# Kernel optimization log

Measured on AMD Instinct MI355X. Metric: run time of the kernel, lower is better.

Reference implementation:

```python
import jax, jax.numpy as jnp
import numpy as np

KAPPA = 5.0
EPS_NORM = 1e-12  # torch F.normalize eps
EPS_LOG = 1e-09


def setup_inputs() -> dict:
    key = jax.random.key(0)
    student_output = jax.random.normal(key, (16384, 256), dtype=jnp.float32)
    return {"student_output": student_output}


def reference(student_output) -> jnp.ndarray:
    # L2-normalize rows (matches F.normalize: x / max(||x||, eps))
    norm = jnp.linalg.norm(student_output, axis=-1, keepdims=True)
    x_norm = student_output / jnp.maximum(norm, EPS_NORM)
    # pairwise cosine similarity [n, n]
    sim = x_norm @ x_norm.T
    kernel = jnp.exp(KAPPA * sim)
    density_estimates = kernel.sum(axis=1)  # [n]
    entropy = -jnp.mean(jnp.log(density_estimates + EPS_LOG))
    return entropy
```

## Files before the change

kernel.cpp:

```cpp
#include <hip/hip_runtime.h>


#define NROWS 16384
#define KDIM 256
#define NTILE 128
#define NT (NROWS / NTILE)
#define NSTRIP 4
#define TOTAL_BLOCKS (NT * NSTRIP)

#define SQRT_KLOG2E 2.68579577857f

typedef int i32x4_t __attribute__((ext_vector_type(4)));
typedef int i32x8_t __attribute__((ext_vector_type(8)));
typedef float f32x16_t __attribute__((ext_vector_type(16)));
typedef __attribute__((address_space(1))) const void global_cvoid_t;
typedef __attribute__((address_space(3))) void lds_void_t;

#if __has_builtin(__builtin_amdgcn_exp2f)
#define EXP2(x) __builtin_amdgcn_exp2f(x)
#else
#define EXP2(x) exp2f(x)
#endif

union frag8 { i32x8_t v8; i32x4_t v4[2]; };

__global__ __launch_bounds__(256)
void kde_normalize(const float* __restrict__ X, unsigned int* __restrict__ Xn8,
                   float* __restrict__ density, unsigned int* __restrict__ ticket) {
  const int wave = threadIdx.x >> 6;
  const int lane = threadIdx.x & 63;
  const int row = blockIdx.x * 4 + wave;
  const float4 v = ((const float4*)(X + (size_t)row * KDIM))[lane];
  float ss = v.x * v.x + v.y * v.y + v.z * v.z + v.w * v.w;
  ss += __shfl_xor(ss, 1);
  ss += __shfl_xor(ss, 2);
  ss += __shfl_xor(ss, 4);
  ss += __shfl_xor(ss, 8);
  ss += __shfl_xor(ss, 16);
  ss += __shfl_xor(ss, 32);
  const float scale = SQRT_KLOG2E / fmaxf(sqrtf(ss), 1e-12f);
  int p = 0;
  p = __builtin_amdgcn_cvt_pk_fp8_f32(v.x * scale, v.y * scale, p, false);
  p = __builtin_amdgcn_cvt_pk_fp8_f32(v.z * scale, v.w * scale, p, true);
  Xn8[(size_t)row * 64 + lane] = (unsigned int)p;
  if (threadIdx.x < 4) density[blockIdx.x * 4 + threadIdx.x] = 0.0f;
  if (blockIdx.x == 0 && threadIdx.x == 0) *ticket = 0u;
}

__global__ __launch_bounds__(512, 4)
void kde_gemm(const unsigned char* __restrict__ Xn8, float* __restrict__ density,
              unsigned int* __restrict__ ticket, float* __restrict__ out) {
  extern __shared__ char smem[];
  char* buf0 = smem;
  char* buf1 = smem + 32768;

  const int tid = threadIdx.x;
  const int wave = tid >> 6;
  const int lane = tid & 63;
  const int wr = wave >> 1;
  const int wc = wave & 1;
  const int m32 = lane & 31;
  const int h = lane >> 5;
  const int bi = blockIdx.x;
  const int s = blockIdx.y;
  const int t0 = s * 16;
  const int nt = (s == 0 && bi < NT / 2) ? 17 : 16;
  const char* Xb = (const char*)Xn8;

#define STAGE(base_row, dst)                                                      \
  for (int c = wave; c < 32; c += 8) {                                            \
    const int rt = c >> 3, kb = (c >> 1) & 3, hh = c & 1;                         \
    const size_t gofs =                                                           \
        (size_t)((base_row) + rt * 32 + m32) * KDIM + kb * 64 + h * 32 + hh * 16; \
    __builtin_amdgcn_global_load_lds((global_cvoid_t*)(Xb + gofs),                \
                                     (lds_void_t*)((dst) + c * 1024), 16, 0, 0);  \
  }

  STAGE(bi * NTILE, buf0);
  STAGE(((bi + t0) & (NT - 1)) * NTILE, buf1);
  __syncthreads();

  frag8 areg[4];
#pragma unroll
  for (int kb = 0; kb < 4; kb++) {
    const char* pa = buf0 + (wr * 8 + kb * 2) * 1024 + lane * 16;
    areg[kb].v4[0] = *(const i32x4_t*)pa;
    areg[kb].v4[1] = *(const i32x4_t*)(pa + 1024);
  }
  __syncthreads();

  float rs[16];
#pragma unroll
  for (int r = 0; r < 16; r++) rs[r] = 0.0f;

  for (int k = 0; k < nt; ++k) {
    const int t = t0 + (k == 16 ? 48 : k) + (k == 16 ? 16 : 0);
    const int J = (bi + t) & (NT - 1);
    char* rbuf = (k & 1) ? buf0 : buf1;
    char* sbuf = (k & 1) ? buf1 : buf0;

    if (k + 1 < nt) {
      const int tn = t0 + (k + 1 == 16 ? 64 : k + 1);
      STAGE(((bi + tn) & (NT - 1)) * NTILE, sbuf);
    }

    f32x16_t acc[2];
#pragma unroll
    for (int j = 0; j < 2; j++) acc[j] = (f32x16_t)0.0f;

#pragma unroll
    for (int kb = 0; kb < 4; ++kb) {
      frag8 bf[2];
#pragma unroll
      for (int j = 0; j < 2; j++) {
        const char* pb = rbuf + ((wc * 2 + j) * 8 + kb * 2) * 1024 + lane * 16;
        bf[j].v4[0] = *(const i32x4_t*)pb;
        bf[j].v4[1] = *(const i32x4_t*)(pb + 1024);
      }
#pragma unroll
      for (int j = 0; j < 2; j++)
        acc[j] = __builtin_amdgcn_mfma_scale_f32_32x32x64_f8f6f4(
            areg[kb].v8, bf[j].v8, acc[j], 0, 0, 0, 127, 0, 127);
    }

    float cs[2] = {0.0f, 0.0f};
#pragma unroll
    for (int j = 0; j < 2; j++)
#pragma unroll
      for (int r = 0; r < 16; r++) {
        const float e = EXP2(acc[j][r]);
        rs[r] += e;
        cs[j] += e;
      }

    if (t != 0) {
#pragma unroll
      for (int j = 0; j < 2; j++) {
        float v = cs[j] + __shfl_xor(cs[j], 32);
        if (h == 0)
          atomicAdd(&density[J * NTILE + wc * 64 + j * 32 + m32], v);
      }
    }

    __syncthreads();
  }

#pragma unroll
  for (int r = 0; r < 16; r++) {
    float v = rs[r];
    v += __shfl_xor(v, 1);
    v += __shfl_xor(v, 2);
    v += __shfl_xor(v, 4);
    v += __shfl_xor(v, 8);
    v += __shfl_xor(v, 16);
    if (m32 == 0) {
      const int row = bi * NTILE + wr * 32 + (r & 3) + 8 * (r >> 2) + 4 * h;
      atomicAdd(&density[row], v);
    }
  }
#undef STAGE

  __syncthreads();
  if (tid == 0) {
    __threadfence();
    ((volatile unsigned int*)smem)[0] = atomicAdd(ticket, 1u);
  }
  __syncthreads();
  if (((volatile unsigned int*)smem)[0] == TOTAL_BLOCKS - 1) {
    __threadfence();
    float ssum = 0.0f;
    for (int i = tid; i < NROWS; i += 512) {
      const float d = __hip_atomic_load(&density[i], __ATOMIC_RELAXED,
                                        __HIP_MEMORY_SCOPE_AGENT);
      ssum += logf(d + 1e-9f);
    }
    ssum += __shfl_xor(ssum, 1);
    ssum += __shfl_xor(ssum, 2);
    ssum += __shfl_xor(ssum, 4);
    ssum += __shfl_xor(ssum, 8);
    ssum += __shfl_xor(ssum, 16);
    ssum += __shfl_xor(ssum, 32);
    float* red = ((float*)smem) + 16;
    if (lane == 0) red[wave] = ssum;
    __syncthreads();
    if (tid == 0) {
      float tot = 0.0f;
      for (int w = 0; w < 8; w++) tot += red[w];
      out[0] = -tot / (float)NROWS;
    }
  }
}

extern "C" void kernel_launch(void* const* d_in, const int* in_sizes, int n_in,
                              void* d_out, int out_size, void* d_ws, size_t ws_size,
                              hipStream_t stream) {
  const float* X = (const float*)d_in[0];
  float* out = (float*)d_out;
  char* ws = (char*)d_ws;
  unsigned int* Xn8 = (unsigned int*)ws;
  float* density = (float*)(ws + (size_t)NROWS * KDIM);
  unsigned int* ticket = (unsigned int*)(density + NROWS);

  hipFuncSetAttribute((const void*)kde_gemm,
                      hipFuncAttributeMaxDynamicSharedMemorySize, 65536);

  kde_normalize<<<NROWS / 4, 256, 0, stream>>>(X, Xn8, density, ticket);
  kde_gemm<<<dim3(NT, NSTRIP), 512, 65536, stream>>>((const unsigned char*)ws,
                                                     density, ticket, out);
}
```

Before: 124.7 us.

## Split tile staging into halves, buffer column sums in LDS, add MFMA priority

Each k-iteration now loads the next tile in two halves. Explicit vmcnt waits and raw barriers replace the full __syncthreads, so loads can overlap the MFMA and exp work. Per-tile column sums accumulate into an LDS buffer with LDS atomics and are flushed to global density once at the end, which removes the per-iteration global atomics. The change also adds s_setprio around the MFMAs and packs the row-sum accumulators as float2, at the cost of extra LDS and more delicate hand-written synchronisation.

```diff
diff --git a/kernel.cpp b/kernel.cpp
--- a/kernel.cpp
+++ b/kernel.cpp
@@ -10,8 +10,12 @@
 
 #define SQRT_KLOG2E 2.68579577857f
 
+#define CS_LDS_FLOATS (17 * NTILE)
+#define SMEM_BYTES (65536 + CS_LDS_FLOATS * 4)
+
 typedef int i32x4_t __attribute__((ext_vector_type(4)));
 typedef int i32x8_t __attribute__((ext_vector_type(8)));
+typedef float f32x2_t __attribute__((ext_vector_type(2)));
 typedef float f32x16_t __attribute__((ext_vector_type(16)));
 typedef __attribute__((address_space(1))) const void global_cvoid_t;
 typedef __attribute__((address_space(3))) void lds_void_t;
@@ -21,6 +25,8 @@
 #else
 #define EXP2(x) exp2f(x)
 #endif
+
+#define WAITVM(n) asm volatile("s_waitcnt vmcnt(" #n ")" ::: "memory")
 
 union frag8 { i32x8_t v8; i32x4_t v4[2]; };
 
@@ -53,6 +59,7 @@
   extern __shared__ char smem[];
   char* buf0 = smem;
   char* buf1 = smem + 32768;
+  float* cs_lds = (float*)(smem + 65536);
 
   const int tid = threadIdx.x;
   const int wave = tid >> 6;
@@ -76,6 +83,22 @@
                                      (lds_void_t*)((dst) + c * 1024), 16, 0, 0);  \
   }
 
+#define STAGE_HALF(base_row, dst, hf)                                             \
+  {                                                                               \
+    const int rt_ = wave >> 1;                                                    \
+    const int kb_ = 2 * (hf) + (wave & 1);                                        \
+    const size_t g0_ =                                                            \
+        (size_t)((base_row) + rt_ * 32 + m32) * KDIM + kb_ * 64 + h * 32;         \
+    __builtin_amdgcn_global_load_lds(                                             \
+        (global_cvoid_t*)(Xb + g0_),                                              \
+        (lds_void_t*)((dst) + (rt_ * 8 + kb_ * 2) * 1024), 16, 0, 0);             \
+    __builtin_amdgcn_global_load_lds(                                             \
+        (global_cvoid_t*)(Xb + g0_ + 16),                                         \
+        (lds_void_t*)((dst) + (rt_ * 8 + kb_ * 2 + 1) * 1024), 16, 0, 0);         \
+  }
+
+  for (int i = tid; i < nt * NTILE; i += 512) cs_lds[i] = 0.0f;
+
   STAGE(bi * NTILE, buf0);
   STAGE(((bi + t0) & (NT - 1)) * NTILE, buf1);
   __syncthreads();
@@ -89,65 +112,87 @@
   }
   __syncthreads();
 
-  float rs[16];
-#pragma unroll
-  for (int r = 0; r < 16; r++) rs[r] = 0.0f;
+  f32x2_t rs2[8];
+#pragma unroll
+  for (int r = 0; r < 8; r++) rs2[r] = (f32x2_t)0.0f;
 
   for (int k = 0; k < nt; ++k) {
-    const int t = t0 + (k == 16 ? 48 : k) + (k == 16 ? 16 : 0);
-    const int J = (bi + t) & (NT - 1);
+    const int t = (k == 16) ? 64 : (t0 + k);
     char* rbuf = (k & 1) ? buf0 : buf1;
     char* sbuf = (k & 1) ? buf1 : buf0;
-
-    if (k + 1 < nt) {
-      const int tn = t0 + (k + 1 == 16 ? 64 : k + 1);
-      STAGE(((bi + tn) & (NT - 1)) * NTILE, sbuf);
-    }
+    const bool pre = (k + 1 < nt);
+    const int tn = (k + 1 == 16) ? 64 : (t0 + k + 1);
+    const int Jn = (bi + tn) & (NT - 1);
 
     f32x16_t acc[2];
 #pragma unroll
     for (int j = 0; j < 2; j++) acc[j] = (f32x16_t)0.0f;
 
-#pragma unroll
-    for (int kb = 0; kb < 4; ++kb) {
+    if (pre) STAGE_HALF(Jn * NTILE, sbuf, 0);
+#pragma unroll
+    for (int kbl = 0; kbl < 2; ++kbl) {
       frag8 bf[2];
 #pragma unroll
       for (int j = 0; j < 2; j++) {
-        const char* pb = rbuf + ((wc * 2 + j) * 8 + kb * 2) * 1024 + lane * 16;
+        const char* pb = rbuf + ((wc * 2 + j) * 8 + kbl * 2) * 1024 + lane * 16;
         bf[j].v4[0] = *(const i32x4_t*)pb;
         bf[j].v4[1] = *(const i32x4_t*)(pb + 1024);
       }
+      __builtin_amdgcn_s_setprio(1);
 #pragma unroll
       for (int j = 0; j < 2; j++)
         acc[j] = __builtin_amdgcn_mfma_scale_f32_32x32x64_f8f6f4(
-            areg[kb].v8, bf[j].v8, acc[j], 0, 0, 0, 127, 0, 127);
-    }
-
-    float cs[2] = {0.0f, 0.0f};
-#pragma unroll
-    for (int j = 0; j < 2; j++)
-#pragma unroll
-      for (int r = 0; r < 16; r++) {
-        const float e = EXP2(acc[j][r]);
-        rs[r] += e;
-        cs[j] += e;
-      }
-
-    if (t != 0) {
+            areg[kbl].v8, bf[j].v8, acc[j], 0, 0, 0, 127, 0, 127);
+      __builtin_amdgcn_s_setprio(0);
+    }
+    if (pre) { WAITVM(2); } else { WAITVM(0); }
+    __builtin_amdgcn_s_barrier();
+
+    if (pre) STAGE_HALF(Jn * NTILE, sbuf, 1);
+#pragma unroll
+    for (int kbl = 0; kbl < 2; ++kbl) {
+      frag8 bf[2];
 #pragma unroll
       for (int j = 0; j < 2; j++) {
-        float v = cs[j] + __shfl_xor(cs[j], 32);
+        const char* pb =
+            rbuf + ((wc * 2 + j) * 8 + (2 + kbl) * 2) * 1024 + lane * 16;
+        bf[j].v4[0] = *(const i32x4_t*)pb;
+        bf[j].v4[1] = *(const i32x4_t*)(pb + 1024);
+      }
+      __builtin_amdgcn_s_setprio(1);
+#pragma unroll
+      for (int j = 0; j < 2; j++)
+        acc[j] = __builtin_amdgcn_mfma_scale_f32_32x32x64_f8f6f4(
+            areg[2 + kbl].v8, bf[j].v8, acc[j], 0, 0, 0, 127, 0, 127);
+      __builtin_amdgcn_s_setprio(0);
+    }
+
+#pragma unroll
+    for (int j = 0; j < 2; j++) {
+      f32x2_t csj = (f32x2_t)0.0f;
+#pragma unroll
+      for (int r2 = 0; r2 < 8; r2++) {
+        f32x2_t e;
+        e.x = EXP2(acc[j][2 * r2]);
+        e.y = EXP2(acc[j][2 * r2 + 1]);
+        rs2[r2] += e;
+        csj += e;
+      }
+      if (t != 0) {
+        float v = csj.x + csj.y;
+        v += __shfl_xor(v, 32);
         if (h == 0)
-          atomicAdd(&density[J * NTILE + wc * 64 + j * 32 + m32], v);
-      }
-    }
-
-    __syncthreads();
+          atomicAdd(&cs_lds[k * NTILE + wc * 64 + j * 32 + m32], v);
+      }
+    }
+
+    if (pre) { WAITVM(2); } else { WAITVM(0); }
+    __builtin_amdgcn_s_barrier();
   }
 
 #pragma unroll
   for (int r = 0; r < 16; r++) {
-    float v = rs[r];
+    float v = rs2[r >> 1][r & 1];
     v += __shfl_xor(v, 1);
     v += __shfl_xor(v, 2);
     v += __shfl_xor(v, 4);
@@ -158,7 +203,17 @@
       atomicAdd(&density[row], v);
     }
   }
+
+  __syncthreads();
+  for (int idx = tid; idx < nt * NTILE; idx += 512) {
+    const int kk = idx >> 7;
+    const int tt = (kk == 16) ? 64 : (t0 + kk);
+    if (tt == 0) continue;
+    const int JJ = (bi + tt) & (NT - 1);
+    atomicAdd(&density[JJ * NTILE + (idx & 127)], cs_lds[idx]);
+  }
 #undef STAGE
+#undef STAGE_HALF
 
   __syncthreads();
   if (tid == 0) {
@@ -202,9 +257,9 @@
   unsigned int* ticket = (unsigned int*)(density + NROWS);
 
   hipFuncSetAttribute((const void*)kde_gemm,
-                      hipFuncAttributeMaxDynamicSharedMemorySize, 65536);
+                      hipFuncAttributeMaxDynamicSharedMemorySize, SMEM_BYTES);
 
   kde_normalize<<<NROWS / 4, 256, 0, stream>>>(X, Xn8, density, ticket);
-  kde_gemm<<<dim3(NT, NSTRIP), 512, 65536, stream>>>((const unsigned char*)ws,
-                                                     density, ticket, out);
+  kde_gemm<<<dim3(NT, NSTRIP), 512, SMEM_BYTES, stream>>>(
+      (const unsigned char*)ws, density, ticket, out);
 }
```

Result: slower. 131.1 us (+5.1%).

## Software-pipeline exp epilogue behind next MFMA tile and batch column sums in LDS

Applied to the files above, without the earlier changes.

Unrolls the tile loop two iterations at a time with ping-pong accumulators, so the exp2/row-sum epilogue of the previous tile is issued alongside the MFMAs of the current tile. Per-tile column sums now go to LDS with atomics, and are flushed to global density with atomics once at the end, replacing per-tile global atomics. Accumulation also uses packed 2-wide float vectors. The cost is a second set of accumulator registers, which may cause spills under the 512-thread, 4-block launch bound, plus about 8.7KB of extra LDS per block.

```diff
diff --git a/kernel.cpp b/kernel.cpp
--- a/kernel.cpp
+++ b/kernel.cpp
@@ -10,8 +10,12 @@
 
 #define SQRT_KLOG2E 2.68579577857f
 
+#define CS_LDS_FLOATS (17 * NTILE)
+#define SMEM_BYTES (65536 + CS_LDS_FLOATS * 4)
+
 typedef int i32x4_t __attribute__((ext_vector_type(4)));
 typedef int i32x8_t __attribute__((ext_vector_type(8)));
+typedef float f32x2_t __attribute__((ext_vector_type(2)));
 typedef float f32x16_t __attribute__((ext_vector_type(16)));
 typedef __attribute__((address_space(1))) const void global_cvoid_t;
 typedef __attribute__((address_space(3))) void lds_void_t;
@@ -53,6 +57,7 @@
   extern __shared__ char smem[];
   char* buf0 = smem;
   char* buf1 = smem + 32768;
+  float* cs_lds = (float*)(smem + 65536);
 
   const int tid = threadIdx.x;
   const int wave = tid >> 6;
@@ -76,6 +81,58 @@
                                      (lds_void_t*)((dst) + c * 1024), 16, 0, 0);  \
   }
 
+#define EPI(ACC, KI)                                                              \
+  {                                                                               \
+    const int tt_ = ((KI) == 16) ? 64 : (t0 + (KI));                              \
+    _Pragma("unroll")                                                             \
+    for (int j = 0; j < 2; j++) {                                                 \
+      f32x2_t csj = (f32x2_t)0.0f;                                                \
+      _Pragma("unroll")                                                           \
+      for (int r2 = 0; r2 < 8; r2++) {                                            \
+        f32x2_t e;                                                                \
+        e.x = EXP2(ACC[j][2 * r2]);                                               \
+        e.y = EXP2(ACC[j][2 * r2 + 1]);                                           \
+        rs2[r2] += e;                                           \
+        csj += e;                                                                 \
+      }                                                                           \
+      if (tt_ != 0) {                       \
+        float v_ = csj.x + csj.y;                                                 \
+        v_ += __shfl_xor(v_, 32);                \
+        if (h == 0)                                                               \
+          atomicAdd(&cs_lds[(KI) * NTILE + wc * 64 + j * 32 + m32], v_);          \
+      }                                                                           \
+    }                                                                             \
+  }
+
+#define BODY(K, PAR, ACCW, ACCR, DO_EPI, KPREV)                                   \
+  {                                                                               \
+    char* rbuf_ = (PAR) ? buf0 : buf1;          \
+    char* sbuf_ = (PAR) ? buf1 : buf0;               \
+    if ((K) + 1 < nt) {                                                           \
+      const int tn_ = ((K) + 1 == 16) ? 64 : (t0 + (K) + 1);                      \
+      STAGE(((bi + tn_) & (NT - 1)) * NTILE, sbuf_);                              \
+    }                                                                             \
+    if (DO_EPI) EPI(ACCR, KPREV);                                                 \
+    _Pragma("unroll")                                                             \
+    for (int kbl = 0; kbl < 4; ++kbl) {                                           \
+      frag8 bf[2];                                                                \
+      _Pragma("unroll")                                                           \
+      for (int j = 0; j < 2; j++) {                                               \
+        const char* pb = rbuf_ + ((wc * 2 + j) * 8 + kbl * 2) * 1024 + lane * 16; \
+        bf[j].v4[0] = *(const i32x4_t*)pb;                                        \
+        bf[j].v4[1] = *(const i32x4_t*)(pb + 1024);                               \
+      }                                                                           \
+      _Pragma("unroll")                                                           \
+      for (int j = 0; j < 2; j++)                                                 \
+        ACCW[j] = __builtin_amdgcn_mfma_scale_f32_32x32x64_f8f6f4(                \
+            areg[kbl].v8, bf[j].v8,                                               \
+            (kbl == 0) ? (f32x16_t)0.0f : ACCW[j], 0, 0, 0, 127, 0, 127);         \
+    }                                                                             \
+    __syncthreads();    \
+  }
+
+  for (int i = tid; i < nt * NTILE; i += 512) cs_lds[i] = 0.0f;
+
   STAGE(bi * NTILE, buf0);
   STAGE(((bi + t0) & (NT - 1)) * NTILE, buf1);
   __syncthreads();
@@ -89,65 +146,29 @@
   }
   __syncthreads();
 
-  float rs[16];
+  f32x2_t rs2[8];
 #pragma unroll
-  for (int r = 0; r < 16; r++) rs[r] = 0.0f;
-
-  for (int k = 0; k < nt; ++k) {
-    const int t = t0 + (k == 16 ? 48 : k) + (k == 16 ? 16 : 0);
-    const int J = (bi + t) & (NT - 1);
-    char* rbuf = (k & 1) ? buf0 : buf1;
-    char* sbuf = (k & 1) ? buf1 : buf0;
-
-    if (k + 1 < nt) {
-      const int tn = t0 + (k + 1 == 16 ? 64 : k + 1);
-      STAGE(((bi + tn) & (NT - 1)) * NTILE, sbuf);
-    }
-
-    f32x16_t acc[2];
-#pragma unroll
-    for (int j = 0; j < 2; j++) acc[j] = (f32x16_t)0.0f;
-
-#pragma unroll
-    for (int kb = 0; kb < 4; ++kb) {
-      frag8 bf[2];
-#pragma unroll
-      for (int j = 0; j < 2; j++) {
-        const char* pb = rbuf + ((wc * 2 + j) * 8 + kb * 2) * 1024 + lane * 16;
-        bf[j].v4[0] = *(const i32x4_t*)pb;
-        bf[j].v4[1] = *(const i32x4_t*)(pb + 1024);
-      }
-#pragma unroll
-      for (int j = 0; j < 2; j++)
-        acc[j] = __builtin_amdgcn_mfma_scale_f32_32x32x64_f8f6f4(
-            areg[kb].v8, bf[j].v8, acc[j], 0, 0, 0, 127, 0, 127);
-    }
-
-    float cs[2] = {0.0f, 0.0f};
-#pragma unroll
-    for (int j = 0; j < 2; j++)
-#pragma unroll
-      for (int r = 0; r < 16; r++) {
-        const float e = EXP2(acc[j][r]);
-        rs[r] += e;
-        cs[j] += e;
-      }
-
-    if (t != 0) {
-#pragma unroll
-      for (int j = 0; j < 2; j++) {
-        float v = cs[j] + __shfl_xor(cs[j], 32);
-        if (h == 0)
-          atomicAdd(&density[J * NTILE + wc * 64 + j * 32 + m32], v);
-      }
-    }
-
-    __syncthreads();
+  for (int r = 0; r < 8; r++) rs2[r] = (f32x2_t)0.0f;
+
+  f32x16_t accA[2], accB[2];
+
+  BODY(0, 0, accA, accA, false, 0);
+
+  int k = 1;
+  for (; k + 1 < nt; k += 2) {
+    BODY(k, 1, accB, accA, true, k - 1);
+    BODY(k + 1, 0, accA, accB, true, k);
+  }
+  if (k < nt) {
+    BODY(k, 1, accB, accA, true, k - 1);
+    EPI(accB, k);
+  } else {
+    EPI(accA, nt - 1);
   }
 
 #pragma unroll
   for (int r = 0; r < 16; r++) {
-    float v = rs[r];
+    float v = rs2[r >> 1][r & 1];
     v += __shfl_xor(v, 1);
     v += __shfl_xor(v, 2);
     v += __shfl_xor(v, 4);
@@ -158,7 +179,18 @@
       atomicAdd(&density[row], v);
     }
   }
+
+  __syncthreads();
+  for (int idx = tid; idx < nt * NTILE; idx += 512) {
+    const int kk = idx >> 7;
+    const int tt = (kk == 16) ? 64 : (t0 + kk);
+    if (tt == 0) continue;
+    const int JJ = (bi + tt) & (NT - 1);
+    atomicAdd(&density[JJ * NTILE + (idx & 127)], cs_lds[idx]);
+  }
 #undef STAGE
+#undef EPI
+#undef BODY
 
   __syncthreads();
   if (tid == 0) {
@@ -202,9 +234,9 @@
   unsigned int* ticket = (unsigned int*)(density + NROWS);
 
   hipFuncSetAttribute((const void*)kde_gemm,
-                      hipFuncAttributeMaxDynamicSharedMemorySize, 65536);
+                      hipFuncAttributeMaxDynamicSharedMemorySize, SMEM_BYTES);
 
   kde_normalize<<<NROWS / 4, 256, 0, stream>>>(X, Xn8, density, ticket);
-  kde_gemm<<<dim3(NT, NSTRIP), 512, 65536, stream>>>((const unsigned char*)ws,
-                                                     density, ticket, out);
+  kde_gemm<<<dim3(NT, NSTRIP), 512, SMEM_BYTES, stream>>>(
+      (const unsigned char*)ws, density, ticket, out);
 }
```

After: 222.2 us. 1.78x slower.

## Switch GEMM to 16x16x128 FP8 MFMA with 16 waves per block

Applied to the files above, without the earlier changes.

Replaces the 32x32x64 scaled FP8 MFMA tiling with 16x16x128 MFMAs and doubles the block to 1024 threads (16 waves), so each wave computes a 16x64 sub-tile with smaller accumulators. It remaps the LDS fragment addressing, the exp2 row and column sum reductions, and the per-column atomics to match the new output layout. The aim is more waves in flight and fewer accumulator registers per wave to hide latency in the exp-heavy epilogue. In exchange it adds more block-wide barriers and shuffles per tile, and any mistake in the remapped LDS offsets would silently corrupt the sums.

```diff
diff --git a/kernel.cpp b/kernel.cpp
--- a/kernel.cpp
+++ b/kernel.cpp
@@ -12,7 +12,8 @@
 
 typedef int i32x4_t __attribute__((ext_vector_type(4)));
 typedef int i32x8_t __attribute__((ext_vector_type(8)));
-typedef float f32x16_t __attribute__((ext_vector_type(16)));
+typedef float f32x2_t __attribute__((ext_vector_type(2)));
+typedef float f32x4_t __attribute__((ext_vector_type(4)));
 typedef __attribute__((address_space(1))) const void global_cvoid_t;
 typedef __attribute__((address_space(3))) void lds_void_t;
 
@@ -22,7 +23,7 @@
 #define EXP2(x) exp2f(x)
 #endif
 
-union frag8 { i32x8_t v8; i32x4_t v4[2]; };
+union frag32 { i32x8_t v8; i32x4_t v4[2]; };
 
 __global__ __launch_bounds__(256)
 void kde_normalize(const float* __restrict__ X, unsigned int* __restrict__ Xn8,
@@ -47,7 +48,7 @@
   if (blockIdx.x == 0 && threadIdx.x == 0) *ticket = 0u;
 }
 
-__global__ __launch_bounds__(512, 4)
+__global__ __launch_bounds__(1024, 8)
 void kde_gemm(const unsigned char* __restrict__ Xn8, float* __restrict__ density,
               unsigned int* __restrict__ ticket, float* __restrict__ out) {
   extern __shared__ char smem[];
@@ -57,6 +58,8 @@
   const int tid = threadIdx.x;
   const int wave = tid >> 6;
   const int lane = tid & 63;
+  const int l16 = lane & 15;
+  const int lg = lane >> 4;
   const int wr = wave >> 1;
   const int wc = wave & 1;
   const int m32 = lane & 31;
@@ -68,7 +71,7 @@
   const char* Xb = (const char*)Xn8;
 
 #define STAGE(base_row, dst)                                                      \
-  for (int c = wave; c < 32; c += 8) {                                            \
+  for (int c = wave; c < 32; c += 16) {                                           \
     const int rt = c >> 3, kb = (c >> 1) & 3, hh = c & 1;                         \
     const size_t gofs =                                                           \
         (size_t)((base_row) + rt * 32 + m32) * KDIM + kb * 64 + h * 32 + hh * 16; \
@@ -80,83 +83,88 @@
   STAGE(((bi + t0) & (NT - 1)) * NTILE, buf1);
   __syncthreads();
 
-  frag8 areg[4];
-#pragma unroll
-  for (int kb = 0; kb < 4; kb++) {
-    const char* pa = buf0 + (wr * 8 + kb * 2) * 1024 + lane * 16;
-    areg[kb].v4[0] = *(const i32x4_t*)pa;
-    areg[kb].v4[1] = *(const i32x4_t*)(pa + 1024);
-  }
-  __syncthreads();
-
-  float rs[16];
-#pragma unroll
-  for (int r = 0; r < 16; r++) rs[r] = 0.0f;
+  const int a_row_off = ((wr >> 1) * 8192) + (((wr & 1) * 16 + l16) * 16);
+  const int k_base = ((lg >> 1) * 2048) + ((lg & 1) * 512);
+  const int b_base = wc * 16384 + l16 * 16 + k_base;
+
+  frag32 areg[2];
+#pragma unroll
+  for (int kq = 0; kq < 2; kq++)
+#pragma unroll
+    for (int p = 0; p < 2; p++)
+      areg[kq].v4[p] =
+          *(const i32x4_t*)(buf0 + a_row_off + k_base + kq * 4096 + p * 1024);
+  __syncthreads();
+
+  f32x2_t rs01 = (f32x2_t)0.0f;
+  f32x2_t rs23 = (f32x2_t)0.0f;
 
   for (int k = 0; k < nt; ++k) {
-    const int t = t0 + (k == 16 ? 48 : k) + (k == 16 ? 16 : 0);
+    const int t = (k == 16) ? 64 : (t0 + k);
     const int J = (bi + t) & (NT - 1);
     char* rbuf = (k & 1) ? buf0 : buf1;
     char* sbuf = (k & 1) ? buf1 : buf0;
 
     if (k + 1 < nt) {
-      const int tn = t0 + (k + 1 == 16 ? 64 : k + 1);
+      const int tn = (k + 1 == 16) ? 64 : (t0 + k + 1);
       STAGE(((bi + tn) & (NT - 1)) * NTILE, sbuf);
     }
 
-    f32x16_t acc[2];
-#pragma unroll
-    for (int j = 0; j < 2; j++) acc[j] = (f32x16_t)0.0f;
-
-#pragma unroll
-    for (int kb = 0; kb < 4; ++kb) {
-      frag8 bf[2];
-#pragma unroll
-      for (int j = 0; j < 2; j++) {
-        const char* pb = rbuf + ((wc * 2 + j) * 8 + kb * 2) * 1024 + lane * 16;
-        bf[j].v4[0] = *(const i32x4_t*)pb;
-        bf[j].v4[1] = *(const i32x4_t*)(pb + 1024);
+    f32x4_t acc[4];
+#pragma unroll
+    for (int ct = 0; ct < 4; ct++) acc[ct] = (f32x4_t)0.0f;
+#pragma unroll
+    for (int ct = 0; ct < 4; ct++) {
+      const char* pb = rbuf + b_base + (ct >> 1) * 8192 + (ct & 1) * 256;
+#pragma unroll
+      for (int kq = 0; kq < 2; kq++) {
+        frag32 bf;
+        bf.v4[0] = *(const i32x4_t*)(pb + kq * 4096);
+        bf.v4[1] = *(const i32x4_t*)(pb + kq * 4096 + 1024);
+        acc[ct] = __builtin_amdgcn_mfma_scale_f32_16x16x128_f8f6f4(
+            areg[kq].v8, bf.v8, acc[ct], 0, 0, 0, 127, 0, 127);
       }
-#pragma unroll
-      for (int j = 0; j < 2; j++)
-        acc[j] = __builtin_amdgcn_mfma_scale_f32_32x32x64_f8f6f4(
-            areg[kb].v8, bf[j].v8, acc[j], 0, 0, 0, 127, 0, 127);
-    }
-
-    float cs[2] = {0.0f, 0.0f};
-#pragma unroll
-    for (int j = 0; j < 2; j++)
-#pragma unroll
-      for (int r = 0; r < 16; r++) {
-        const float e = EXP2(acc[j][r]);
-        rs[r] += e;
-        cs[j] += e;
-      }
-
+    }
+
+    float cst[4];
+#pragma unroll
+    for (int ct = 0; ct < 4; ct++) {
+      f32x2_t e01, e23;
+      e01.x = EXP2(acc[ct][0]);
+      e01.y = EXP2(acc[ct][1]);
+      e23.x = EXP2(acc[ct][2]);
+      e23.y = EXP2(acc[ct][3]);
+      rs01 += e01;
+      rs23 += e23;
+      float cs = (e01.x + e01.y) + (e23.x + e23.y);
+      cs += __shfl_xor(cs, 16);
+      cs += __shfl_xor(cs, 32);
+      cst[ct] = cs;
+    }
     if (t != 0) {
-#pragma unroll
-      for (int j = 0; j < 2; j++) {
-        float v = cs[j] + __shfl_xor(cs[j], 32);
-        if (h == 0)
-          atomicAdd(&density[J * NTILE + wc * 64 + j * 32 + m32], v);
-      }
+      const float v = (lg & 2) ? ((lg & 1) ? cst[3] : cst[2])
+                               : ((lg & 1) ? cst[1] : cst[0]);
+      atomicAdd(&density[J * NTILE + wc * 64 + lane], v);
     }
 
     __syncthreads();
   }
 
-#pragma unroll
-  for (int r = 0; r < 16; r++) {
-    float v = rs[r];
-    v += __shfl_xor(v, 1);
-    v += __shfl_xor(v, 2);
-    v += __shfl_xor(v, 4);
-    v += __shfl_xor(v, 8);
-    v += __shfl_xor(v, 16);
-    if (m32 == 0) {
-      const int row = bi * NTILE + wr * 32 + (r & 3) + 8 * (r >> 2) + 4 * h;
-      atomicAdd(&density[row], v);
-    }
+  {
+    float rsv[4] = {rs01.x, rs01.y, rs23.x, rs23.y};
+#pragma unroll
+    for (int r = 0; r < 4; r++) {
+      float v = rsv[r];
+      v += __shfl_xor(v, 1);
+      v += __shfl_xor(v, 2);
+      v += __shfl_xor(v, 4);
+      v += __shfl_xor(v, 8);
+      rsv[r] = v;
+    }
+    const float v = (l16 & 2) ? ((l16 & 1) ? rsv[3] : rsv[2])
+                              : ((l16 & 1) ? rsv[1] : rsv[0]);
+    if (l16 < 4)
+      atomicAdd(&density[bi * NTILE + wr * 16 + lg * 4 + l16], v);
   }
 #undef STAGE
 
@@ -169,7 +177,7 @@
   if (((volatile unsigned int*)smem)[0] == TOTAL_BLOCKS - 1) {
     __threadfence();
     float ssum = 0.0f;
-    for (int i = tid; i < NROWS; i += 512) {
+    for (int i = tid; i < NROWS; i += 1024) {
       const float d = __hip_atomic_load(&density[i], __ATOMIC_RELAXED,
                                         __HIP_MEMORY_SCOPE_AGENT);
       ssum += logf(d + 1e-9f);
@@ -185,7 +193,7 @@
     __syncthreads();
     if (tid == 0) {
       float tot = 0.0f;
-      for (int w = 0; w < 8; w++) tot += red[w];
+      for (int w = 0; w < 16; w++) tot += red[w];
       out[0] = -tot / (float)NROWS;
     }
   }
@@ -205,6 +213,6 @@
                       hipFuncAttributeMaxDynamicSharedMemorySize, 65536);
 
   kde_normalize<<<NROWS / 4, 256, 0, stream>>>(X, Xn8, density, ticket);
-  kde_gemm<<<dim3(NT, NSTRIP), 512, 65536, stream>>>((const unsigned char*)ws,
-                                                     density, ticket, out);
+  kde_gemm<<<dim3(NT, NSTRIP), 1024, 65536, stream>>>((const unsigned char*)ws,
+                                                      density, ticket, out);
 }
```

Result: no change. 124.8 us (+0.0%).
